# Kernel tuning notes

Hardware: AMD Instinct MI355X
Metric: run time of the kernel (lower is better)

## Reference

```python
import jax, jax.numpy as jnp
import numpy as np

HEADSIZE = 64  # per-head feature size (attention dim)
KSIZE, STRIDE, PAD = 3, 1, 1


def setup_inputs() -> dict:
    key = jax.random.key(0)
    k1, k2, k3 = jax.random.split(key, 3)
    B, C, T, H, W = 2, 128, 16, 28, 28
    heads = C // HEADSIZE  # 2
    x = jax.random.normal(k1, (B, C, T, H, W), jnp.float32)
    # learned aggregator query (TokenAggregator, size=1), xavier-normal-ish scale
    q = jax.random.normal(k2, (heads, 1, HEADSIZE), jnp.float32) * (2.0 / (1 + HEADSIZE)) ** 0.5
    # output channel projection (MultiHeadLinear-style, heads=1)
    W_out = jax.random.normal(k3, (C, C), jnp.float32) * (2.0 / (C + C)) ** 0.5
    b_out = jnp.zeros((C,), jnp.float32)
    return {"x": x, "q": q, "W_out": W_out, "b_out": b_out}


def _unfold3d(x, k, s, p):
    # torch unfold-via-identity-conv3d equivalent: [B,C,T,H,W] -> [B,C,k^3,To,Ho,Wo]
    B, C, T, H, W = x.shape
    xp = jnp.pad(x, ((0, 0), (0, 0), (p, p), (p, p), (p, p)))
    To = (T + 2 * p - k) // s + 1
    Ho = (H + 2 * p - k) // s + 1
    Wo = (W + 2 * p - k) // s + 1
    taps = []
    for i in range(k):
        for j in range(k):
            for l in range(k):
                taps.append(xp[:, :, i:i + To * s:s, j:j + Ho * s:s, l:l + Wo * s:s])
    return jnp.stack(taps, axis=2)  # [B, C, K, To, Ho, Wo], K = k^3


def reference(x, q, W_out, b_out):
    patches = _unfold3d(x, KSIZE, STRIDE, PAD)          # [B, C, K, To, Ho, Wo]
    B, C, K, To, Ho, Wo = patches.shape
    hs = HEADSIZE
    heads = C // hs
    # tokenize: per spatial location, K window taps are tokens with C channels
    t = patches.transpose(0, 3, 4, 5, 2, 1)             # [B, To, Ho, Wo, K, C]
    # split_heads(headsize): channel dim C -> (headsize slow, heads fast)
    th = t.reshape(B, To, Ho, Wo, K, hs, heads)         # [..., K, hs, heads]
    scale = hs ** -0.5
    # qkv_aggregate: scale applied to BOTH q and k (effective 1/d), softmax over taps
    logits = jnp.einsum('hoc,btuvkch->btuvhok', q * scale, th * scale)  # [B,To,Ho,Wo,heads,1,K]
    attn = jax.nn.softmax(logits, axis=-1)
    res = jnp.einsum('btuvhok,btuvkch->btuvhoc', attn, th)              # [B,To,Ho,Wo,heads,1,hs]
    # merge_heads: channel order (hs slow, head fast) matches the split ordering
    merged = res[:, :, :, :, :, 0, :].transpose(0, 1, 2, 3, 5, 4).reshape(B, To, Ho, Wo, hs * heads)
    # output channel projection
    y = merged @ W_out.T + b_out                         # [B, To, Ho, Wo, C]
    return y.transpose(0, 4, 1, 2, 3)                    # [B, C, To, Ho, Wo]
```

## Files before the change

kernel.cpp:

```cpp
#include <hip/hip_runtime.h>


#define TT 16
#define HH 28
#define WW 28
#define CC 128
#define SP (TT * HH * WW)
#define NPOS (2 * SP)
#define HS 64
#define KT 27
#define MTS 136

typedef __attribute__((ext_vector_type(8))) short bf16x8;
typedef __attribute__((ext_vector_type(4))) float f32x4;

__device__ __forceinline__ unsigned short bf16_rtne(float f) {
    unsigned u = __float_as_uint(f);
    unsigned r = (u + 0x7FFFu + ((u >> 16) & 1u)) >> 16;
    return (unsigned short)r;
}

__global__ __launch_bounds__(256) void qfield_kernel(
    const float* __restrict__ x, const float* __restrict__ q,
    float* __restrict__ s)
{
    __shared__ float sp[16][32];
    const int tid = threadIdx.x;
    const int pl  = tid & 31;
    const int g   = tid >> 5;
    const int p   = blockIdx.x * 32 + pl;
    const int b   = p / SP;
    const int si  = p % SP;
    const float* xb = x + (size_t)b * CC * SP + si;

    float acc0 = 0.f, acc1 = 0.f;
    #pragma unroll
    for (int j = 0; j < 16; ++j) {
        const int c = g * 16 + j;
        const float val = xb[(size_t)c * SP];
        const float qv  = q[(c & 1) * HS + (c >> 1)] * (1.0f / 64.0f);
        if (c & 1) acc1 += qv * val; else acc0 += qv * val;
    }
    sp[g][pl]     = acc0;
    sp[8 + g][pl] = acc1;
    __syncthreads();
    if (tid < 64) {
        const int h = tid >> 5, pp = tid & 31;
        float a = 0.f;
        #pragma unroll
        for (int g2 = 0; g2 < 8; ++g2) a += sp[h * 8 + g2][pp];
        s[h * NPOS + blockIdx.x * 32 + pp] = a;
    }
}

__global__ __launch_bounds__(256) void awwprep_kernel(
    const float* __restrict__ s, float* __restrict__ aw,
    const float* __restrict__ Wout, unsigned short* __restrict__ Wb)
{
    if (blockIdx.x >= 196) {
        const int i = (blockIdx.x - 196) * 256 + threadIdx.x;
        Wb[i] = bf16_rtne(Wout[i]);
        return;
    }
    const int idx = blockIdx.x * 256 + threadIdx.x;
    const int p = idx % SP;
    const int h = (idx / SP) & 1;
    const int b = idx / (2 * SP);
    const int v = p % WW, u = (p / WW) % HH, t = p / (WW * HH);
    const float* sf = s + h * NPOS + b * SP;

    float l[KT], msk[KT];
    #pragma unroll
    for (int k = 0; k < KT; ++k) {
        const int dt = k / 9 - 1, du = (k / 3) % 3 - 1, dv = k % 3 - 1;
        const int tt = t + dt, uu = u + du, vv = v + dv;
        const bool ok = (unsigned)tt < TT && (unsigned)uu < HH && (unsigned)vv < WW;
        l[k]   = ok ? sf[(tt * HH + uu) * WW + vv] : 0.f;
        msk[k] = ok ? 1.f : 0.f;
    }
    float m = l[0];
    #pragma unroll
    for (int k = 1; k < KT; ++k) m = fmaxf(m, l[k]);
    float sum = 0.f;
    #pragma unroll
    for (int k = 0; k < KT; ++k) { l[k] = __expf(l[k] - m); sum += l[k]; }
    const float inv = 1.f / sum;
    float* awp = aw + (size_t)(b * 2 + h) * KT * SP + p;
    #pragma unroll
    for (int k = 0; k < KT; ++k)
        awp[(size_t)k * SP] = l[k] * inv * msk[k];
}

__global__ __launch_bounds__(256) void fusedmp_kernel(
    const float* __restrict__ x, const float* __restrict__ aw,
    const unsigned short* __restrict__ Wb, const float* __restrict__ bout,
    float* __restrict__ out)
{
    __shared__ unsigned short s_mt[32][MTS];

    const int pb  = (blockIdx.x & 7) * 98 + (blockIdx.x >> 3);
    const int b   = pb / (SP / 32);
    const int p0  = (pb % (SP / 32)) * 32;
    const int tid = threadIdx.x;

    {
        const int cg  = tid >> 3;
        const int p4g = tid & 7;
        const int p   = p0 + p4g * 4;
        const int v0  = p % WW;
        const int u   = (p / WW) % HH;
        const int t   = p / (WW * HH);
        const int h   = cg & 1;
        const float* awp = aw + (size_t)(b * 2 + h) * KT * SP + p;
        const float* xc0 = x + (size_t)(b * CC + cg) * SP;
        const int vl = (v0 == 0)  ? 0  : v0 - 1;
        const int vr = (v0 == 24) ? 27 : v0 + 4;

        float4 acc[4] = { make_float4(0.f,0.f,0.f,0.f), make_float4(0.f,0.f,0.f,0.f),
                          make_float4(0.f,0.f,0.f,0.f), make_float4(0.f,0.f,0.f,0.f) };

        #pragma unroll
        for (int dt = -1; dt <= 1; ++dt) {
            #pragma unroll
            for (int du = -1; du <= 1; ++du) {
                const int tt = t + dt, uu = u + du;
                const bool rok = ((unsigned)tt < TT) && ((unsigned)uu < HH);
                const int rbase = rok ? (tt * HH + uu) * WW : 0;
                const int kb = ((dt + 1) * 3 + (du + 1)) * 3;
                const float4 wm = *(const float4*)&awp[(size_t)(kb + 0) * SP];
                const float4 w0 = *(const float4*)&awp[(size_t)(kb + 1) * SP];
                const float4 wp = *(const float4*)&awp[(size_t)(kb + 2) * SP];
                #pragma unroll
                for (int ci = 0; ci < 4; ++ci) {
                    const float* xc = xc0 + (size_t)(32 * ci) * SP;
                    const float4 a  = *(const float4*)&xc[rbase + v0];
                    const float  xl = xc[rbase + vl];
                    const float  xr = xc[rbase + vr];
                    acc[ci].x += wm.x * xl;  acc[ci].y += wm.y * a.x;
                    acc[ci].z += wm.z * a.y; acc[ci].w += wm.w * a.z;
                    acc[ci].x += w0.x * a.x; acc[ci].y += w0.y * a.y;
                    acc[ci].z += w0.z * a.z; acc[ci].w += w0.w * a.w;
                    acc[ci].x += wp.x * a.y; acc[ci].y += wp.y * a.z;
                    acc[ci].z += wp.z * a.w; acc[ci].w += wp.w * xr;
                }
            }
        }
        #pragma unroll
        for (int ci = 0; ci < 4; ++ci) {
            const int c = cg + 32 * ci;
            s_mt[p4g * 4 + 0][c] = bf16_rtne(acc[ci].x);
            s_mt[p4g * 4 + 1][c] = bf16_rtne(acc[ci].y);
            s_mt[p4g * 4 + 2][c] = bf16_rtne(acc[ci].z);
            s_mt[p4g * 4 + 3][c] = bf16_rtne(acc[ci].w);
        }
    }
    __syncthreads();

    const int w    = tid >> 6;
    const int lane = tid & 63;
    const int lr   = lane & 15;
    const int lk   = lane >> 4;

    #pragma unroll
    for (int ci2 = 0; ci2 < 2; ++ci2) {
        const int cot = w * 2 + ci2;
        const int cob = cot * 16 + lk * 4;
        f32x4 acc0, acc1;
        #pragma unroll
        for (int r = 0; r < 4; ++r) { acc0[r] = bout[cob + r]; acc1[r] = acc0[r]; }

        #pragma unroll
        for (int ks = 0; ks < 4; ++ks) {
            const bf16x8 aA = *(const bf16x8*)&Wb[(size_t)(cot * 16 + lr) * CC + ks * 32 + lk * 8];
            const bf16x8 b0 = *(const bf16x8*)&s_mt[lr     ][ks * 32 + lk * 8];
            const bf16x8 b1 = *(const bf16x8*)&s_mt[16 + lr][ks * 32 + lk * 8];
            acc0 = __builtin_amdgcn_mfma_f32_16x16x32_bf16(aA, b0, acc0, 0, 0, 0);
            acc1 = __builtin_amdgcn_mfma_f32_16x16x32_bf16(aA, b1, acc1, 0, 0, 0);
        }
        const size_t ob = (size_t)b * CC * SP + p0;
        #pragma unroll
        for (int r = 0; r < 4; ++r) {
            out[ob + (size_t)(cob + r) * SP + lr]      = acc0[r];
            out[ob + (size_t)(cob + r) * SP + 16 + lr] = acc1[r];
        }
    }
}

extern "C" void kernel_launch(void* const* d_in, const int* in_sizes, int n_in,
                              void* d_out, int out_size, void* d_ws, size_t ws_size,
                              hipStream_t stream) {
    const float* x    = (const float*)d_in[0];
    const float* q    = (const float*)d_in[1];
    const float* Wout = (const float*)d_in[2];
    const float* bout = (const float*)d_in[3];
    float* out = (float*)d_out;

    float* s  = (float*)d_ws;
    float* aw = s + NPOS;
    unsigned short* Wb = (unsigned short*)(aw + (size_t)4 * KT * SP);

    qfield_kernel <<<dim3(NPOS / 32),     dim3(256), 0, stream>>>(x, q, s);
    awwprep_kernel<<<dim3(196 + 64),      dim3(256), 0, stream>>>(s, aw, Wout, Wb);
    fusedmp_kernel<<<dim3(2 * (SP / 32)), dim3(256), 0, stream>>>(x, aw, Wb, bout, out);
}
```

Measured before the change: 48.26 us.

## Fuse softmax weight computation into main kernel and merge weight conversion into qfield

The separate softmax kernel that wrote 27 attention weights per position and head to global memory is removed. Each block of the main kernel now computes those weights for its 32 positions into shared memory using 64 threads, and the bf16 conversion of the output projection moves into the qfield launch. This drops one kernel launch and the large global write and read of the weight buffer. In exchange the main kernel gains a serial prologue that only a quarter of its threads execute, plus an extra barrier.

```diff
diff --git a/kernel.cpp b/kernel.cpp
--- a/kernel.cpp
+++ b/kernel.cpp
@@ -20,10 +20,16 @@
     return (unsigned short)r;
 }
 
-__global__ __launch_bounds__(256) void qfield_kernel(
+__global__ __launch_bounds__(256) void qfieldw_kernel(
     const float* __restrict__ x, const float* __restrict__ q,
-    float* __restrict__ s)
+    float* __restrict__ s,
+    const float* __restrict__ Wout, unsigned short* __restrict__ Wb)
 {
+    if (blockIdx.x >= 784) {
+        const int i = (blockIdx.x - 784) * 256 + threadIdx.x;
+        Wb[i] = bf16_rtne(Wout[i]);
+        return;
+    }
     __shared__ float sp[16][32];
     const int tid = threadIdx.x;
     const int pl  = tid & 31;
@@ -53,55 +59,46 @@
     }
 }
 
-__global__ __launch_bounds__(256) void awwprep_kernel(
-    const float* __restrict__ s, float* __restrict__ aw,
-    const float* __restrict__ Wout, unsigned short* __restrict__ Wb)
-{
-    if (blockIdx.x >= 196) {
-        const int i = (blockIdx.x - 196) * 256 + threadIdx.x;
-        Wb[i] = bf16_rtne(Wout[i]);
-        return;
-    }
-    const int idx = blockIdx.x * 256 + threadIdx.x;
-    const int p = idx % SP;
-    const int h = (idx / SP) & 1;
-    const int b = idx / (2 * SP);
-    const int v = p % WW, u = (p / WW) % HH, t = p / (WW * HH);
-    const float* sf = s + h * NPOS + b * SP;
-
-    float l[KT], msk[KT];
-    #pragma unroll
-    for (int k = 0; k < KT; ++k) {
-        const int dt = k / 9 - 1, du = (k / 3) % 3 - 1, dv = k % 3 - 1;
-        const int tt = t + dt, uu = u + du, vv = v + dv;
-        const bool ok = (unsigned)tt < TT && (unsigned)uu < HH && (unsigned)vv < WW;
-        l[k]   = ok ? sf[(tt * HH + uu) * WW + vv] : 0.f;
-        msk[k] = ok ? 1.f : 0.f;
-    }
-    float m = l[0];
-    #pragma unroll
-    for (int k = 1; k < KT; ++k) m = fmaxf(m, l[k]);
-    float sum = 0.f;
-    #pragma unroll
-    for (int k = 0; k < KT; ++k) { l[k] = __expf(l[k] - m); sum += l[k]; }
-    const float inv = 1.f / sum;
-    float* awp = aw + (size_t)(b * 2 + h) * KT * SP + p;
-    #pragma unroll
-    for (int k = 0; k < KT; ++k)
-        awp[(size_t)k * SP] = l[k] * inv * msk[k];
-}
-
 __global__ __launch_bounds__(256) void fusedmp_kernel(
-    const float* __restrict__ x, const float* __restrict__ aw,
+    const float* __restrict__ x, const float* __restrict__ s,
     const unsigned short* __restrict__ Wb, const float* __restrict__ bout,
     float* __restrict__ out)
 {
+    __shared__ float s_aw[KT][2][32];
     __shared__ unsigned short s_mt[32][MTS];
 
     const int pb  = (blockIdx.x & 7) * 98 + (blockIdx.x >> 3);
     const int b   = pb / (SP / 32);
     const int p0  = (pb % (SP / 32)) * 32;
     const int tid = threadIdx.x;
+
+    if (tid < 64) {
+        const int h  = tid >> 5;
+        const int pl = tid & 31;
+        const int p  = p0 + pl;
+        const int v = p % WW, u = (p / WW) % HH, t = p / (WW * HH);
+        const float* sf = s + h * NPOS + b * SP;
+        float l[KT], msk[KT];
+        #pragma unroll
+        for (int k = 0; k < KT; ++k) {
+            const int dt = k / 9 - 1, du = (k / 3) % 3 - 1, dv = k % 3 - 1;
+            const int tt = t + dt, uu = u + du, vv = v + dv;
+            const bool ok = (unsigned)tt < TT && (unsigned)uu < HH && (unsigned)vv < WW;
+            l[k]   = ok ? sf[(tt * HH + uu) * WW + vv] : 0.f;
+            msk[k] = ok ? 1.f : 0.f;
+        }
+        float m = l[0];
+        #pragma unroll
+        for (int k = 1; k < KT; ++k) m = fmaxf(m, l[k]);
+        float sum = 0.f;
+        #pragma unroll
+        for (int k = 0; k < KT; ++k) { l[k] = __expf(l[k] - m); sum += l[k]; }
+        const float inv = 1.f / sum;
+        #pragma unroll
+        for (int k = 0; k < KT; ++k)
+            s_aw[k][h][pl] = l[k] * inv * msk[k];
+    }
+    __syncthreads();
 
     {
         const int cg  = tid >> 3;
@@ -111,7 +108,6 @@
         const int u   = (p / WW) % HH;
         const int t   = p / (WW * HH);
         const int h   = cg & 1;
-        const float* awp = aw + (size_t)(b * 2 + h) * KT * SP + p;
         const float* xc0 = x + (size_t)(b * CC + cg) * SP;
         const int vl = (v0 == 0)  ? 0  : v0 - 1;
         const int vr = (v0 == 24) ? 27 : v0 + 4;
@@ -127,9 +123,9 @@
                 const bool rok = ((unsigned)tt < TT) && ((unsigned)uu < HH);
                 const int rbase = rok ? (tt * HH + uu) * WW : 0;
                 const int kb = ((dt + 1) * 3 + (du + 1)) * 3;
-                const float4 wm = *(const float4*)&awp[(size_t)(kb + 0) * SP];
-                const float4 w0 = *(const float4*)&awp[(size_t)(kb + 1) * SP];
-                const float4 wp = *(const float4*)&awp[(size_t)(kb + 2) * SP];
+                const float4 wm = *(const float4*)&s_aw[kb + 0][h][p4g * 4];
+                const float4 w0 = *(const float4*)&s_aw[kb + 1][h][p4g * 4];
+                const float4 wp = *(const float4*)&s_aw[kb + 2][h][p4g * 4];
                 #pragma unroll
                 for (int ci = 0; ci < 4; ++ci) {
                     const float* xc = xc0 + (size_t)(32 * ci) * SP;
@@ -195,11 +191,9 @@
     const float* bout = (const float*)d_in[3];
     float* out = (float*)d_out;
 
-    float* s  = (float*)d_ws;
-    float* aw = s + NPOS;
-    unsigned short* Wb = (unsigned short*)(aw + (size_t)4 * KT * SP);
+    float* s = (float*)d_ws;
+    unsigned short* Wb = (unsigned short*)(s + 2 * NPOS);
 
-    qfield_kernel <<<dim3(NPOS / 32),     dim3(256), 0, stream>>>(x, q, s);
-    awwprep_kernel<<<dim3(196 + 64),      dim3(256), 0, stream>>>(s, aw, Wout, Wb);
-    fusedmp_kernel<<<dim3(2 * (SP / 32)), dim3(256), 0, stream>>>(x, aw, Wb, bout, out);
+    qfieldw_kernel<<<dim3(784 + 64),      dim3(256), 0, stream>>>(x, q, s, Wout, Wb);
+    fusedmp_kernel<<<dim3(2 * (SP / 32)), dim3(256), 0, stream>>>(x, s, Wb, bout, out);
 }
```

Result: faster. 44.53 us (-7.7%).
